# Performance work log

Measured on AMD Instinct MI355X. Metric: run time of the kernel, lower is better.

The kernel has to match this reference:

```python
import jax, jax.numpy as jnp
import numpy as np

B, S, D = 2, 2048, 1024
H, DK, DV = 16, 64, 64


def setup_inputs() -> dict:
    key = jax.random.key(0)
    ks = jax.random.split(key, 10)
    scale = 0.02
    return {
        "x": jax.random.normal(ks[0], (B, S, D), dtype=jnp.float32),
        "Wq": jax.random.normal(ks[1], (D, H * DK), dtype=jnp.float32) * scale,
        "bq": jax.random.normal(ks[2], (H * DK,), dtype=jnp.float32) * scale,
        "Wk": jax.random.normal(ks[3], (D, H * DK), dtype=jnp.float32) * scale,
        "bk": jax.random.normal(ks[4], (H * DK,), dtype=jnp.float32) * scale,
        "Wv": jax.random.normal(ks[5], (D, H * DV), dtype=jnp.float32) * scale,
        "bv": jax.random.normal(ks[6], (H * DV,), dtype=jnp.float32) * scale,
        "Wo": jax.random.normal(ks[7], (H * DV, D), dtype=jnp.float32) * scale,
        "bo": jax.random.normal(ks[8], (D,), dtype=jnp.float32) * scale,
    }


def reference(x, Wq, bq, Wk, bk, Wv, bv, Wo, bo):
    b, s, d = x.shape
    # projections -> (b, H, s, dk/dv)
    q = (x @ Wq + bq).reshape(b, s, H, DK).transpose(0, 2, 1, 3)
    k = (x @ Wk + bk).reshape(b, s, H, DK).transpose(0, 2, 1, 3)
    v = (x @ Wv + bv).reshape(b, s, H, DV).transpose(0, 2, 1, 3)
    # scaled QK^T: (b, H, s, s)
    scores = jnp.einsum("bhqd,bhkd->bhqk", q, k) / np.sqrt(DK).astype(np.float32)
    # sign-based reweighting: scores * sign(scores) (zeros -> sign 1) == |scores|
    reweighted = jnp.abs(scores)
    # causal mask: lower triangle keeps value, strict upper -> -inf (value * -inf)
    causal = jnp.tril(jnp.ones((s, s), dtype=bool))
    logits = jnp.where(causal, reweighted, -jnp.inf)
    w = jax.nn.softmax(logits, axis=-1)
    o = jnp.einsum("bhqk,bhkd->bhqd", w, v)  # (b, H, s, DV)
    o = o.transpose(0, 2, 1, 3).reshape(b, s, H * DV)
    return o @ Wo + bo
```

## Files before the change

kernel.cpp:

```cpp
#include <hip/hip_runtime.h>


#define DI __device__ __forceinline__

typedef __bf16 bf16x8 __attribute__((ext_vector_type(8)));
typedef float f32x4 __attribute__((ext_vector_type(4)));
typedef unsigned short u16x8 __attribute__((ext_vector_type(8)));
typedef unsigned short u16x4 __attribute__((ext_vector_type(4)));

union U8 { u16x8 u; bf16x8 b; };
union PB { unsigned int w[4]; u16x8 u; bf16x8 b; };

typedef const __attribute__((address_space(1))) unsigned int* gas_p;
typedef __attribute__((address_space(3))) unsigned int* las_p;

DI void gload16(const unsigned short* g, unsigned short* l) {
  __builtin_amdgcn_global_load_lds((gas_p)(const void*)g, (las_p)(void*)l, 16, 0, 0);
}

#define WAIT_VM4  asm volatile("s_waitcnt vmcnt(4)" ::: "memory")
#define WAIT_VM0  asm volatile("s_waitcnt vmcnt(0)" ::: "memory")
#define WAIT_LGKM asm volatile("s_waitcnt lgkmcnt(0)" ::: "memory")
#define BARRIER   __builtin_amdgcn_s_barrier()

DI unsigned short f2bf(float f) {
  unsigned int u = __float_as_uint(f);
  u += 0x7FFFu + ((u >> 16) & 1u);
  return (unsigned short)(u >> 16);
}
DI float bf2f(unsigned short v) { return __uint_as_float((unsigned int)v << 16); }

__global__ __launch_bounds__(256) void k_conv_x(const float* __restrict__ x,
                                                unsigned short* __restrict__ xb) {
  size_t i = ((size_t)blockIdx.x * 256 + threadIdx.x) * 4;
  float4 v = *(const float4*)(x + i);
  u16x4 o;
  o[0] = f2bf(v.x); o[1] = f2bf(v.y); o[2] = f2bf(v.z); o[3] = f2bf(v.w);
  *(u16x4*)(xb + i) = o;
}

__global__ __launch_bounds__(256) void k_transpose(
    const float* __restrict__ W0, const float* __restrict__ W1,
    const float* __restrict__ W2, const float* __restrict__ W3,
    unsigned short* __restrict__ T0, unsigned short* __restrict__ T1,
    unsigned short* __restrict__ T2, unsigned short* __restrict__ T3) {
  const int z = blockIdx.z;
  const float* W = (z == 0) ? W0 : (z == 1) ? W1 : (z == 2) ? W2 : W3;
  unsigned short* T = (z == 0) ? T0 : (z == 1) ? T1 : (z == 2) ? T2 : T3;
  __shared__ unsigned short buf[32][33];
  const int k0 = blockIdx.x * 32, n0 = blockIdx.y * 32;
  const int tx = threadIdx.x, ty = threadIdx.y;
#pragma unroll
  for (int j = 0; j < 4; ++j) {
    int r = ty + j * 8;
    buf[r][tx] = f2bf(W[(size_t)(k0 + r) * 1024 + n0 + tx]);
  }
  __syncthreads();
#pragma unroll
  for (int j = 0; j < 4; ++j) {
    int c = ty + j * 8;
    T[(size_t)(n0 + c) * 1024 + k0 + tx] = buf[tx][c];
  }
}

DI void stage_gemm(const unsigned short* __restrict__ src, unsigned short* dst,
                   int row0, int k0, int tid, int wid) {
#pragma unroll
  for (int i = 0; i < 2; ++i) {
    int T = i * 256 + tid;
    int row = T >> 2, ch = T & 3;
    int sch = ch ^ (row & 3);
    gload16(&src[(size_t)(row0 + row) * 1024 + k0 + sch * 8],
            &dst[(i * 256 + wid * 64) * 8]);
  }
}

DI void gemm_main(const unsigned short* __restrict__ A,
                  const unsigned short* __restrict__ Bm,
                  unsigned short* As, unsigned short* Bs,
                  int m0, int n0, f32x4 acc[4][4]) {
  const int tid = threadIdx.x;
  const int lane = tid & 63, wid = tid >> 6;
  const int wr = wid >> 1, wc = wid & 1;
  const int g = lane >> 4, lq = lane & 15;

  stage_gemm(A, As, m0, 0, tid, wid);
  stage_gemm(Bm, Bs, n0, 0, tid, wid);
  __syncthreads();
  int buf = 0;
  for (int k0 = 0; k0 < 1024; k0 += 32) {
    if (k0 + 32 < 1024) {
      stage_gemm(A, As + (buf ^ 1) * 4096, m0, k0 + 32, tid, wid);
      stage_gemm(Bm, Bs + (buf ^ 1) * 4096, n0, k0 + 32, tid, wid);
    }
    const unsigned short* Ab = As + buf * 4096;
    const unsigned short* Bb = Bs + buf * 4096;
    U8 af[4], bfr[4];
#pragma unroll
    for (int f = 0; f < 4; ++f) {
      af[f].u  = *(const u16x8*)&Ab[(wr * 64 + f * 16 + lq) * 32 + ((g ^ (lq & 3)) * 8)];
      bfr[f].u = *(const u16x8*)&Bb[(wc * 64 + f * 16 + lq) * 32 + ((g ^ (lq & 3)) * 8)];
    }
#pragma unroll
    for (int i = 0; i < 4; ++i)
#pragma unroll
      for (int j = 0; j < 4; ++j)
        acc[i][j] = __builtin_amdgcn_mfma_f32_16x16x32_bf16(af[i].b, bfr[j].b,
                                                            acc[i][j], 0, 0, 0);
    __syncthreads();
    buf ^= 1;
  }
}

__global__ __launch_bounds__(256) void k_gemm_qkv(
    const unsigned short* __restrict__ xb,
    const unsigned short* __restrict__ Wqt, const unsigned short* __restrict__ Wkt,
    const unsigned short* __restrict__ Wvt,
    const float* __restrict__ bq, const float* __restrict__ bk,
    const float* __restrict__ bv,
    unsigned short* __restrict__ Qo, unsigned short* __restrict__ Ko,
    unsigned short* __restrict__ Vto) {
  __shared__ unsigned short Sh[128 * 136];
  unsigned short* As = Sh;
  unsigned short* Bs = Sh + 8192;
  const int z = blockIdx.z;
  const unsigned short* Bm = (z == 0) ? Wqt : (z == 1) ? Wkt : Wvt;
  const float* bias = (z == 0) ? bq : (z == 1) ? bk : bv;

  f32x4 acc[4][4];
#pragma unroll
  for (int i = 0; i < 4; ++i)
#pragma unroll
    for (int j = 0; j < 4; ++j) acc[i][j] = f32x4{0.f, 0.f, 0.f, 0.f};

  const int m0 = blockIdx.x * 128, n0 = blockIdx.y * 128;
  gemm_main(xb, Bm, As, Bs, m0, n0, acc);

  const int tid = threadIdx.x;
  const int lane = tid & 63, wid = tid >> 6;
  const int wr = wid >> 1, wc = wid & 1;
  const int g = lane >> 4, lq = lane & 15;
  const int bb = m0 >> 11;

#pragma unroll
  for (int j = 0; j < 4; ++j) {
    int col = wc * 64 + j * 16 + lq;
    float bv_ = bias[n0 + col];
#pragma unroll
    for (int i = 0; i < 4; ++i)
#pragma unroll
      for (int r = 0; r < 4; ++r) {
        int row = wr * 64 + i * 16 + g * 4 + r;
        Sh[row * 136 + col] = f2bf(acc[i][j][r] + bv_);
      }
  }
  __syncthreads();

  if (z < 2) {
    unsigned short* dstQK = (z == 0) ? Qo : Ko;
    const int ch = tid & 15, sb = tid >> 4;
#pragma unroll
    for (int it = 0; it < 8; ++it) {
      int s = sb + it * 16;
      u16x8 v = *(const u16x8*)&Sh[s * 136 + ch * 8];
      int gcol = n0 + ch * 8;
      int hh = gcol >> 6, dd = gcol & 63;
      int sr = (m0 + s) & 2047;
      *(u16x8*)&dstQK[(((size_t)(bb * 16 + hh)) * 2048 + sr) * 64 + dd] = v;
    }
  } else {
    const int d = tid & 127, hf = tid >> 7;
    int gcol = n0 + d;
    int hh = gcol >> 6, dd = gcol & 63;
    size_t vrow = ((size_t)(bb * 16 + hh)) * 64 + dd;
#pragma unroll
    for (int it = 0; it < 8; ++it) {
      int s0 = (hf + it * 2) * 8;
      u16x8 vv;
#pragma unroll
      for (int e = 0; e < 8; ++e) vv[e] = Sh[(s0 + e) * 136 + d];
      *(u16x8*)&Vto[vrow * 2048 + (m0 & 2047) + s0] = vv;
    }
  }
}

__global__ __launch_bounds__(256) void k_gemm_out(
    const unsigned short* __restrict__ Ob, const unsigned short* __restrict__ Wot,
    const float* __restrict__ bo, float* __restrict__ out) {
  __shared__ unsigned short As[2 * 4096];
  __shared__ unsigned short Bs[2 * 4096];
  f32x4 acc[4][4];
#pragma unroll
  for (int i = 0; i < 4; ++i)
#pragma unroll
    for (int j = 0; j < 4; ++j) acc[i][j] = f32x4{0.f, 0.f, 0.f, 0.f};

  const int m0 = blockIdx.x * 128, n0 = blockIdx.y * 128;
  gemm_main(Ob, Wot, As, Bs, m0, n0, acc);

  const int lane = threadIdx.x & 63, wid = threadIdx.x >> 6;
  const int wr = wid >> 1, wc = wid & 1;
  const int g = lane >> 4, lq = lane & 15;
#pragma unroll
  for (int j = 0; j < 4; ++j) {
    int col = n0 + wc * 64 + j * 16 + lq;
    float bv_ = bo[col];
#pragma unroll
    for (int i = 0; i < 4; ++i)
#pragma unroll
      for (int r = 0; r < 4; ++r) {
        int row = m0 + wr * 64 + i * 16 + g * 4 + r;
        out[(size_t)row * 1024 + col] = acc[i][j][r] + bv_;
      }
  }
}

template<bool MASKED>
DI void ptile(f32x4 sacc[4], f32x4& lacc, unsigned int pk[4][2], int qloc, int g) {
  const float SC = 0.18033688011112042f;
#pragma unroll
  for (int c = 0; c < 4; ++c) {
#pragma unroll
    for (int r = 0; r < 4; ++r) {
      float sv = fabsf(sacc[c][r]) * SC;
      if (MASKED) {
        int k = g * 8 + r + 4 * (c & 1) + 32 * (c >> 1);
        sv = (k <= qloc) ? sv : -1e30f;
      }
      float p = exp2f(sv);
      sacc[c][r] = p;
      lacc[r] += p;
    }
    asm("v_cvt_pk_bf16_f32 %0, %1, %2"
        : "=v"(pk[c][0]) : "v"(sacc[c][0]), "v"(sacc[c][1]));
    asm("v_cvt_pk_bf16_f32 %0, %1, %2"
        : "=v"(pk[c][1]) : "v"(sacc[c][2]), "v"(sacc[c][3]));
  }
}

DI void flash_one(bool complete, int qblk, int t0, int t1, int slot,
                  const unsigned short* __restrict__ Q,
                  const unsigned short* __restrict__ Km,
                  const unsigned short* __restrict__ Vt,
                  unsigned short* __restrict__ O,
                  unsigned short* __restrict__ Pp, float* __restrict__ Lp,
                  unsigned short* Ks0, unsigned short* Vs0,
                  size_t qkbase, size_t vbase, int b, int h,
                  int tid, int wid, int g, int lq) {
  const int qloc = wid * 16 + lq;
  const int qrow = qblk * 64 + qloc;

  auto stage = [&](int bf, int t) {
    const int kk0 = t * 64;
#pragma unroll
    for (int i = 0; i < 2; ++i) {
      int T = i * 256 + tid;
      int row = T >> 3, ch = T & 7;
      int sch = ch ^ (row & 7);
      gload16(&Km[qkbase + (size_t)(kk0 + row) * 64 + sch * 8],
              Ks0 + bf * 4096 + (i * 2048 + wid * 512));
      gload16(&Vt[vbase + (size_t)row * 2048 + kk0 + sch * 8],
              Vs0 + bf * 4096 + (i * 2048 + wid * 512));
    }
  };

  U8 aq0, aq1;
  {
    const unsigned short* qp = &Q[qkbase + (size_t)qrow * 64 + g * 8];
    aq0.u = *(const u16x8*)qp;
    aq1.u = *(const u16x8*)(qp + 32);
  }
  f32x4 lacc = f32x4{0.f, 0.f, 0.f, 0.f};
  f32x4 oacc[4];
#pragma unroll
  for (int c = 0; c < 4; ++c) oacc[c] = f32x4{0.f, 0.f, 0.f, 0.f};

  const int rbase = (lq >> 2) * 8 + (lq & 3);

  stage(0, t0);
  if (t0 + 1 < t1) stage(1, t0 + 1);
  int buf = 0;
  for (int t = t0; t < t1; ++t) {
    if (t + 1 < t1) WAIT_VM4; else WAIT_VM0;
    BARRIER;
    const unsigned short* Kb = Ks0 + buf * 4096;
    const unsigned short* Vb = Vs0 + buf * 4096;
    f32x4 sacc[4];
    __builtin_amdgcn_s_setprio(1);
#pragma unroll
    for (int c = 0; c < 4; ++c) {
      int row = rbase + 4 * (c & 1) + 32 * (c >> 1);
      int r7 = row & 7;
      U8 kf0, kf1;
      kf0.u = *(const u16x8*)&Kb[row * 64 + ((g ^ r7) * 8)];
      kf1.u = *(const u16x8*)&Kb[row * 64 + (((4 + g) ^ r7) * 8)];
      sacc[c] = __builtin_amdgcn_mfma_f32_16x16x32_bf16(kf0.b, aq0.b,
                                                        f32x4{0.f, 0.f, 0.f, 0.f}, 0, 0, 0);
      sacc[c] = __builtin_amdgcn_mfma_f32_16x16x32_bf16(kf1.b, aq1.b, sacc[c], 0, 0, 0);
    }
    __builtin_amdgcn_s_setprio(0);
    unsigned int pk[4][2];
    if (t == qblk) ptile<true>(sacc, lacc, pk, qloc, g);
    else           ptile<false>(sacc, lacc, pk, qloc, g);
    __builtin_amdgcn_s_setprio(1);
#pragma unroll
    for (int hh = 0; hh < 2; ++hh) {
      PB pb;
      pb.w[0] = pk[hh * 2 + 0][0];
      pb.w[1] = pk[hh * 2 + 0][1];
      pb.w[2] = pk[hh * 2 + 1][0];
      pb.w[3] = pk[hh * 2 + 1][1];
#pragma unroll
      for (int c = 0; c < 4; ++c) {
        U8 vf;
        vf.u = *(const u16x8*)&Vb[(c * 16 + lq) * 64 + (((hh * 4 + g) ^ (lq & 7)) * 8)];
        oacc[c] = __builtin_amdgcn_mfma_f32_16x16x32_bf16(vf.b, pb.b, oacc[c], 0, 0, 0);
      }
    }
    __builtin_amdgcn_s_setprio(0);
    WAIT_LGKM;
    BARRIER;
    if (t + 2 < t1) stage(buf, t + 2);
    buf ^= 1;
  }

  float ls = (lacc[0] + lacc[1]) + (lacc[2] + lacc[3]);
  ls += __shfl_xor(ls, 16, 64);
  ls += __shfl_xor(ls, 32, 64);
  if (complete) {
    float inv_l = 1.0f / ls;
#pragma unroll
    for (int c = 0; c < 4; ++c) {
      u16x4 ov;
#pragma unroll
      for (int r2 = 0; r2 < 4; ++r2) ov[r2] = f2bf(oacc[c][r2] * inv_l);
      *(u16x4*)&O[((size_t)(b * 2048 + qrow)) * 1024 + h * 64 + c * 16 + g * 4] = ov;
    }
  } else {
    if (g == 0) Lp[slot * 64 + qloc] = ls;
    size_t pbase = (size_t)slot * 4096 + qloc * 64;
#pragma unroll
    for (int c = 0; c < 4; ++c) {
      u16x4 ov;
#pragma unroll
      for (int r2 = 0; r2 < 4; ++r2) ov[r2] = f2bf(oacc[c][r2]);
      *(u16x4*)&Pp[pbase + c * 16 + g * 4] = ov;
    }
  }
}

__global__ __launch_bounds__(256) void k_flash(
    const unsigned short* __restrict__ Q, const unsigned short* __restrict__ Km,
    const unsigned short* __restrict__ Vt, unsigned short* __restrict__ O,
    unsigned short* __restrict__ Pp, float* __restrict__ Lp) {
  __shared__ unsigned short Ks[2 * 4096];
  __shared__ unsigned short Vs[2 * 4096];
  const int tid = threadIdx.x;
  const int lane = tid & 63, wid = tid >> 6;
  const int g = lane >> 4, lq = lane & 15;
  const int bid = blockIdx.x;
  const int xcd = bid & 7, r = bid >> 3;
  const int bh = xcd * 4 + (r >> 5);
  const int rr = r & 31;
  const int p = rr >> 1, sp = rr & 1;
  const int mq = 31 - p, mi = 15 - p;
  const int b = bh >> 4, h = bh & 15;
  const size_t qkbase = (size_t)bh * 2048 * 64;
  const size_t vbase = (size_t)bh * 64 * 2048;

  if (sp == 0) {
    flash_one(true, p, 0, p + 1, 0, Q, Km, Vt, O, Pp, Lp,
              Ks, Vs, qkbase, vbase, b, h, tid, wid, g, lq);
    flash_one(false, mq, 0, 16 - p, (bh * 16 + mi) * 2 + 0, Q, Km, Vt, O, Pp, Lp,
              Ks, Vs, qkbase, vbase, b, h, tid, wid, g, lq);
  } else {
    flash_one(false, mq, 16 - p, 32 - p, (bh * 16 + mi) * 2 + 1, Q, Km, Vt, O, Pp, Lp,
              Ks, Vs, qkbase, vbase, b, h, tid, wid, g, lq);
  }
}

__global__ __launch_bounds__(256) void k_combine(
    const unsigned short* __restrict__ Pp, const float* __restrict__ Lp,
    unsigned short* __restrict__ O) {
  int gid = blockIdx.x * 256 + threadIdx.x;
  int dv4 = gid & 15;
  int q   = (gid >> 4) & 63;
  int mi  = (gid >> 10) & 15;
  int bh  = gid >> 14;
  int pairbase = (bh * 16 + mi) * 2;
  size_t base = (size_t)pairbase * 4096 + q * 64 + dv4 * 4;
  u16x4 a = *(const u16x4*)&Pp[base];
  u16x4 c = *(const u16x4*)&Pp[base + 4096];
  float l = Lp[pairbase * 64 + q] + Lp[(pairbase + 1) * 64 + q];
  float inv = 1.0f / l;
  u16x4 o;
#pragma unroll
  for (int r = 0; r < 4; ++r) o[r] = f2bf((bf2f(a[r]) + bf2f(c[r])) * inv);
  int b = bh >> 4, h = bh & 15;
  int srow = (mi + 16) * 64 + q;
  *(u16x4*)&O[((size_t)(b * 2048 + srow)) * 1024 + h * 64 + dv4 * 4] = o;
}

extern "C" void kernel_launch(void* const* d_in, const int* in_sizes, int n_in,
                              void* d_out, int out_size, void* d_ws, size_t ws_size,
                              hipStream_t stream) {
  const float* x  = (const float*)d_in[0];
  const float* Wq = (const float*)d_in[1];
  const float* bq = (const float*)d_in[2];
  const float* Wk = (const float*)d_in[3];
  const float* bk = (const float*)d_in[4];
  const float* Wv = (const float*)d_in[5];
  const float* bv = (const float*)d_in[6];
  const float* Wo = (const float*)d_in[7];
  const float* bo = (const float*)d_in[8];
  float* out = (float*)d_out;

  char* ws = (char*)d_ws;
  const size_t MB = 1024 * 1024;
  unsigned short* xb   = (unsigned short*)(ws + 0 * MB);
  unsigned short* Wqt  = (unsigned short*)(ws + 8 * MB);
  unsigned short* Wkt  = (unsigned short*)(ws + 10 * MB);
  unsigned short* Wvt  = (unsigned short*)(ws + 12 * MB);
  unsigned short* Wot  = (unsigned short*)(ws + 14 * MB);
  unsigned short* Qws  = (unsigned short*)(ws + 16 * MB);
  unsigned short* Kws  = (unsigned short*)(ws + 24 * MB);
  unsigned short* Vtws = (unsigned short*)(ws + 32 * MB);
  unsigned short* Ows  = (unsigned short*)(ws + 40 * MB);
  unsigned short* Pp   = (unsigned short*)(ws + 0 * MB);
  float*          Lp   = (float*)(ws + 8 * MB);

  k_conv_x<<<4096, 256, 0, stream>>>(x, xb);
  k_transpose<<<dim3(32, 32, 4), dim3(32, 8), 0, stream>>>(Wq, Wk, Wv, Wo,
                                                           Wqt, Wkt, Wvt, Wot);
  k_gemm_qkv<<<dim3(32, 8, 3), 256, 0, stream>>>(xb, Wqt, Wkt, Wvt, bq, bk, bv,
                                                 Qws, Kws, Vtws);
  k_flash<<<1024, 256, 0, stream>>>(Qws, Kws, Vtws, Ows, Pp, Lp);
  k_combine<<<2048, 256, 0, stream>>>(Pp, Lp, Ows);
  k_gemm_out<<<dim3(32, 8), 256, 0, stream>>>(Ows, Wot, bo, out);
}
```

Measured before the change: 113.5 us.

## Process two 16-row query tiles per wave to reuse K/V fragments in flash attention

Each wave now handles 32 query rows (128 per block) rather than 16, so every K and V fragment read from LDS feeds two MFMAs and each staged K/V tile serves twice as many queries. The causal load-balancing pairing and the split-partial combine layout are adjusted for 128-row query blocks, and the flash grid is halved to 512 blocks. This cuts LDS and global K/V traffic per query. In exchange it raises register pressure, halves the number of blocks (fewer waves to hide latency), and applies masking to two diagonal tiles per block.

```diff
diff --git a/kernel.cpp b/kernel.cpp
--- a/kernel.cpp
+++ b/kernel.cpp
@@ -216,7 +216,8 @@
 }
 
 template<bool MASKED>
-DI void ptile(f32x4 sacc[4], f32x4& lacc, unsigned int pk[4][2], int qloc, int g) {
+DI void ptile(f32x4 sacc[4], f32x4& lacc, unsigned int pk[4][2],
+              int qrow, int kk0, int g) {
   const float SC = 0.18033688011112042f;
 #pragma unroll
   for (int c = 0; c < 4; ++c) {
@@ -224,8 +225,8 @@
     for (int r = 0; r < 4; ++r) {
       float sv = fabsf(sacc[c][r]) * SC;
       if (MASKED) {
-        int k = g * 8 + r + 4 * (c & 1) + 32 * (c >> 1);
-        sv = (k <= qloc) ? sv : -1e30f;
+        int k = kk0 + g * 8 + r + 4 * (c & 1) + 32 * (c >> 1);
+        sv = (k <= qrow) ? sv : -1e30f;
       }
       float p = exp2f(sv);
       sacc[c][r] = p;
@@ -238,17 +239,18 @@
   }
 }
 
-DI void flash_one(bool complete, int qblk, int t0, int t1, int slot,
-                  const unsigned short* __restrict__ Q,
-                  const unsigned short* __restrict__ Km,
-                  const unsigned short* __restrict__ Vt,
-                  unsigned short* __restrict__ O,
-                  unsigned short* __restrict__ Pp, float* __restrict__ Lp,
-                  unsigned short* Ks0, unsigned short* Vs0,
-                  size_t qkbase, size_t vbase, int b, int h,
-                  int tid, int wid, int g, int lq) {
-  const int qloc = wid * 16 + lq;
-  const int qrow = qblk * 64 + qloc;
+DI void flash_dual(bool complete, int qblk, int t0, int t1, int slot,
+                   const unsigned short* __restrict__ Q,
+                   const unsigned short* __restrict__ Km,
+                   const unsigned short* __restrict__ Vt,
+                   unsigned short* __restrict__ O,
+                   unsigned short* __restrict__ Pp, float* __restrict__ Lp,
+                   unsigned short* Ks0, unsigned short* Vs0,
+                   size_t qkbase, size_t vbase, int b, int h,
+                   int tid, int wid, int g, int lq) {
+  const int lrowA = wid * 32 + lq, lrowB = lrowA + 16;
+  const int qrowA = qblk * 128 + lrowA, qrowB = qblk * 128 + lrowB;
+  const int diag0 = 2 * qblk;
 
   auto stage = [&](int bf, int t) {
     const int kk0 = t * 64;
@@ -264,16 +266,22 @@
     }
   };
 
-  U8 aq0, aq1;
+  U8 aqA0, aqA1, aqB0, aqB1;
   {
-    const unsigned short* qp = &Q[qkbase + (size_t)qrow * 64 + g * 8];
-    aq0.u = *(const u16x8*)qp;
-    aq1.u = *(const u16x8*)(qp + 32);
-  }
-  f32x4 lacc = f32x4{0.f, 0.f, 0.f, 0.f};
-  f32x4 oacc[4];
-#pragma unroll
-  for (int c = 0; c < 4; ++c) oacc[c] = f32x4{0.f, 0.f, 0.f, 0.f};
+    const unsigned short* qp = &Q[qkbase + (size_t)qrowA * 64 + g * 8];
+    aqA0.u = *(const u16x8*)qp;
+    aqA1.u = *(const u16x8*)(qp + 32);
+    const unsigned short* qp2 = &Q[qkbase + (size_t)qrowB * 64 + g * 8];
+    aqB0.u = *(const u16x8*)qp2;
+    aqB1.u = *(const u16x8*)(qp2 + 32);
+  }
+  f32x4 laccA = f32x4{0.f, 0.f, 0.f, 0.f}, laccB = f32x4{0.f, 0.f, 0.f, 0.f};
+  f32x4 oaccA[4], oaccB[4];
+#pragma unroll
+  for (int c = 0; c < 4; ++c) {
+    oaccA[c] = f32x4{0.f, 0.f, 0.f, 0.f};
+    oaccB[c] = f32x4{0.f, 0.f, 0.f, 0.f};
+  }
 
   const int rbase = (lq >> 2) * 8 + (lq & 3);
 
@@ -285,7 +293,8 @@
     BARRIER;
     const unsigned short* Kb = Ks0 + buf * 4096;
     const unsigned short* Vb = Vs0 + buf * 4096;
-    f32x4 sacc[4];
+    const int kk0 = t * 64;
+    f32x4 saccA[4], saccB[4];
     __builtin_amdgcn_s_setprio(1);
 #pragma unroll
     for (int c = 0; c < 4; ++c) {
@@ -294,27 +303,36 @@
       U8 kf0, kf1;
       kf0.u = *(const u16x8*)&Kb[row * 64 + ((g ^ r7) * 8)];
       kf1.u = *(const u16x8*)&Kb[row * 64 + (((4 + g) ^ r7) * 8)];
-      sacc[c] = __builtin_amdgcn_mfma_f32_16x16x32_bf16(kf0.b, aq0.b,
-                                                        f32x4{0.f, 0.f, 0.f, 0.f}, 0, 0, 0);
-      sacc[c] = __builtin_amdgcn_mfma_f32_16x16x32_bf16(kf1.b, aq1.b, sacc[c], 0, 0, 0);
+      saccA[c] = __builtin_amdgcn_mfma_f32_16x16x32_bf16(kf0.b, aqA0.b,
+                                                         f32x4{0.f, 0.f, 0.f, 0.f}, 0, 0, 0);
+      saccA[c] = __builtin_amdgcn_mfma_f32_16x16x32_bf16(kf1.b, aqA1.b, saccA[c], 0, 0, 0);
+      saccB[c] = __builtin_amdgcn_mfma_f32_16x16x32_bf16(kf0.b, aqB0.b,
+                                                         f32x4{0.f, 0.f, 0.f, 0.f}, 0, 0, 0);
+      saccB[c] = __builtin_amdgcn_mfma_f32_16x16x32_bf16(kf1.b, aqB1.b, saccB[c], 0, 0, 0);
     }
     __builtin_amdgcn_s_setprio(0);
-    unsigned int pk[4][2];
-    if (t == qblk) ptile<true>(sacc, lacc, pk, qloc, g);
-    else           ptile<false>(sacc, lacc, pk, qloc, g);
+    unsigned int pkA[4][2], pkB[4][2];
+    if (t >= diag0) {
+      ptile<true>(saccA, laccA, pkA, qrowA, kk0, g);
+      ptile<true>(saccB, laccB, pkB, qrowB, kk0, g);
+    } else {
+      ptile<false>(saccA, laccA, pkA, qrowA, kk0, g);
+      ptile<false>(saccB, laccB, pkB, qrowB, kk0, g);
+    }
     __builtin_amdgcn_s_setprio(1);
 #pragma unroll
     for (int hh = 0; hh < 2; ++hh) {
-      PB pb;
-      pb.w[0] = pk[hh * 2 + 0][0];
-      pb.w[1] = pk[hh * 2 + 0][1];
-      pb.w[2] = pk[hh * 2 + 1][0];
-      pb.w[3] = pk[hh * 2 + 1][1];
+      PB pbA, pbB;
+      pbA.w[0] = pkA[hh * 2 + 0][0]; pbA.w[1] = pkA[hh * 2 + 0][1];
+      pbA.w[2] = pkA[hh * 2 + 1][0]; pbA.w[3] = pkA[hh * 2 + 1][1];
+      pbB.w[0] = pkB[hh * 2 + 0][0]; pbB.w[1] = pkB[hh * 2 + 0][1];
+      pbB.w[2] = pkB[hh * 2 + 1][0]; pbB.w[3] = pkB[hh * 2 + 1][1];
 #pragma unroll
       for (int c = 0; c < 4; ++c) {
         U8 vf;
         vf.u = *(const u16x8*)&Vb[(c * 16 + lq) * 64 + (((hh * 4 + g) ^ (lq & 7)) * 8)];
-        oacc[c] = __builtin_amdgcn_mfma_f32_16x16x32_bf16(vf.b, pb.b, oacc[c], 0, 0, 0);
+        oaccA[c] = __builtin_amdgcn_mfma_f32_16x16x32_bf16(vf.b, pbA.b, oaccA[c], 0, 0, 0);
+        oaccB[c] = __builtin_amdgcn_mfma_f32_16x16x32_bf16(vf.b, pbB.b, oaccB[c], 0, 0, 0);
       }
     }
     __builtin_amdgcn_s_setprio(0);
@@ -324,27 +342,41 @@
     buf ^= 1;
   }
 
-  float ls = (lacc[0] + lacc[1]) + (lacc[2] + lacc[3]);
-  ls += __shfl_xor(ls, 16, 64);
-  ls += __shfl_xor(ls, 32, 64);
+  float lsA = (laccA[0] + laccA[1]) + (laccA[2] + laccA[3]);
+  lsA += __shfl_xor(lsA, 16, 64);
+  lsA += __shfl_xor(lsA, 32, 64);
+  float lsB = (laccB[0] + laccB[1]) + (laccB[2] + laccB[3]);
+  lsB += __shfl_xor(lsB, 16, 64);
+  lsB += __shfl_xor(lsB, 32, 64);
   if (complete) {
-    float inv_l = 1.0f / ls;
+    float invA = 1.0f / lsA, invB = 1.0f / lsB;
 #pragma unroll
     for (int c = 0; c < 4; ++c) {
-      u16x4 ov;
-#pragma unroll
-      for (int r2 = 0; r2 < 4; ++r2) ov[r2] = f2bf(oacc[c][r2] * inv_l);
-      *(u16x4*)&O[((size_t)(b * 2048 + qrow)) * 1024 + h * 64 + c * 16 + g * 4] = ov;
+      u16x4 ovA, ovB;
+#pragma unroll
+      for (int r2 = 0; r2 < 4; ++r2) {
+        ovA[r2] = f2bf(oaccA[c][r2] * invA);
+        ovB[r2] = f2bf(oaccB[c][r2] * invB);
+      }
+      *(u16x4*)&O[((size_t)(b * 2048 + qrowA)) * 1024 + h * 64 + c * 16 + g * 4] = ovA;
+      *(u16x4*)&O[((size_t)(b * 2048 + qrowB)) * 1024 + h * 64 + c * 16 + g * 4] = ovB;
     }
   } else {
-    if (g == 0) Lp[slot * 64 + qloc] = ls;
-    size_t pbase = (size_t)slot * 4096 + qloc * 64;
+    if (g == 0) {
+      Lp[slot * 128 + lrowA] = lsA;
+      Lp[slot * 128 + lrowB] = lsB;
+    }
+    size_t pbase = (size_t)slot * 8192;
 #pragma unroll
     for (int c = 0; c < 4; ++c) {
-      u16x4 ov;
-#pragma unroll
-      for (int r2 = 0; r2 < 4; ++r2) ov[r2] = f2bf(oacc[c][r2]);
-      *(u16x4*)&Pp[pbase + c * 16 + g * 4] = ov;
+      u16x4 ovA, ovB;
+#pragma unroll
+      for (int r2 = 0; r2 < 4; ++r2) {
+        ovA[r2] = f2bf(oaccA[c][r2]);
+        ovB[r2] = f2bf(oaccB[c][r2]);
+      }
+      *(u16x4*)&Pp[pbase + lrowA * 64 + c * 16 + g * 4] = ovA;
+      *(u16x4*)&Pp[pbase + lrowB * 64 + c * 16 + g * 4] = ovB;
     }
   }
 }
@@ -359,23 +391,23 @@
   const int lane = tid & 63, wid = tid >> 6;
   const int g = lane >> 4, lq = lane & 15;
   const int bid = blockIdx.x;
-  const int xcd = bid & 7, r = bid >> 3;
-  const int bh = xcd * 4 + (r >> 5);
-  const int rr = r & 31;
+  const int xcd = bid & 7, idx = bid >> 3;
+  const int bh = xcd * 4 + (idx >> 4);
+  const int rr = idx & 15;
   const int p = rr >> 1, sp = rr & 1;
-  const int mq = 31 - p, mi = 15 - p;
+  const int mp = 15 - p;
   const int b = bh >> 4, h = bh & 15;
   const size_t qkbase = (size_t)bh * 2048 * 64;
   const size_t vbase = (size_t)bh * 64 * 2048;
 
   if (sp == 0) {
-    flash_one(true, p, 0, p + 1, 0, Q, Km, Vt, O, Pp, Lp,
-              Ks, Vs, qkbase, vbase, b, h, tid, wid, g, lq);
-    flash_one(false, mq, 0, 16 - p, (bh * 16 + mi) * 2 + 0, Q, Km, Vt, O, Pp, Lp,
-              Ks, Vs, qkbase, vbase, b, h, tid, wid, g, lq);
+    flash_dual(true, p, 0, 2 * p + 2, 0, Q, Km, Vt, O, Pp, Lp,
+               Ks, Vs, qkbase, vbase, b, h, tid, wid, g, lq);
+    flash_dual(false, mp, 0, 15 - 2 * p, (bh * 8 + p) * 2 + 0, Q, Km, Vt, O, Pp, Lp,
+               Ks, Vs, qkbase, vbase, b, h, tid, wid, g, lq);
   } else {
-    flash_one(false, mq, 16 - p, 32 - p, (bh * 16 + mi) * 2 + 1, Q, Km, Vt, O, Pp, Lp,
-              Ks, Vs, qkbase, vbase, b, h, tid, wid, g, lq);
+    flash_dual(false, mp, 15 - 2 * p, 32 - 2 * p, (bh * 8 + p) * 2 + 1, Q, Km, Vt, O, Pp, Lp,
+               Ks, Vs, qkbase, vbase, b, h, tid, wid, g, lq);
   }
 }
 
@@ -384,20 +416,20 @@
     unsigned short* __restrict__ O) {
   int gid = blockIdx.x * 256 + threadIdx.x;
   int dv4 = gid & 15;
-  int q   = (gid >> 4) & 63;
-  int mi  = (gid >> 10) & 15;
+  int q   = (gid >> 4) & 127;
+  int pi  = (gid >> 11) & 7;
   int bh  = gid >> 14;
-  int pairbase = (bh * 16 + mi) * 2;
-  size_t base = (size_t)pairbase * 4096 + q * 64 + dv4 * 4;
+  int slot0 = (bh * 8 + pi) * 2;
+  size_t base = (size_t)slot0 * 8192 + q * 64 + dv4 * 4;
   u16x4 a = *(const u16x4*)&Pp[base];
-  u16x4 c = *(const u16x4*)&Pp[base + 4096];
-  float l = Lp[pairbase * 64 + q] + Lp[(pairbase + 1) * 64 + q];
+  u16x4 c = *(const u16x4*)&Pp[base + 8192];
+  float l = Lp[slot0 * 128 + q] + Lp[(slot0 + 1) * 128 + q];
   float inv = 1.0f / l;
   u16x4 o;
 #pragma unroll
   for (int r = 0; r < 4; ++r) o[r] = f2bf((bf2f(a[r]) + bf2f(c[r])) * inv);
   int b = bh >> 4, h = bh & 15;
-  int srow = (mi + 16) * 64 + q;
+  int srow = (15 - pi) * 128 + q;
   *(u16x4*)&O[((size_t)(b * 2048 + srow)) * 1024 + h * 64 + dv4 * 4] = o;
 }
 
@@ -434,7 +466,7 @@
                                                            Wqt, Wkt, Wvt, Wot);
   k_gemm_qkv<<<dim3(32, 8, 3), 256, 0, stream>>>(xb, Wqt, Wkt, Wvt, bq, bk, bv,
                                                  Qws, Kws, Vtws);
-  k_flash<<<1024, 256, 0, stream>>>(Qws, Kws, Vtws, Ows, Pp, Lp);
+  k_flash<<<512, 256, 0, stream>>>(Qws, Kws, Vtws, Ows, Pp, Lp);
   k_combine<<<2048, 256, 0, stream>>>(Pp, Lp, Ows);
   k_gemm_out<<<dim3(32, 8), 256, 0, stream>>>(Ows, Wot, bo, out);
 }
```

After: 111.1 us. -2.1%, faster.
